# Optimization experiments

Hardware: AMD Instinct MI355X
Metric: run time of the kernel (lower is better)

The kernel has to match this reference:

```python
import jax, jax.numpy as jnp
import numpy as np

DEPTH, HEADS, DIM, MLP = 4, 8, 256, 1024
EPS = 1e-5


def setup_inputs() -> dict:
    key = jax.random.key(0)
    ks = jax.random.split(key, 12)
    s = 0.02
    return {
        "x": jax.random.normal(ks[0], (4, 2048, DIM), dtype=jnp.float32),
        "ln1_g": jnp.ones((DEPTH, DIM), jnp.float32),
        "ln1_b": jnp.zeros((DEPTH, DIM), jnp.float32),
        "w_qkv": jax.random.normal(ks[1], (DEPTH, DIM, 3 * DIM), jnp.float32) * s,
        "w_out": jax.random.normal(ks[2], (DEPTH, DIM, DIM), jnp.float32) * s,
        "b_out": jnp.zeros((DEPTH, DIM), jnp.float32),
        "ln2_g": jnp.ones((DEPTH, DIM), jnp.float32),
        "ln2_b": jnp.zeros((DEPTH, DIM), jnp.float32),
        "w1": jax.random.normal(ks[3], (DEPTH, DIM, MLP), jnp.float32) * s,
        "b1": jnp.zeros((DEPTH, MLP), jnp.float32),
        "w2": jax.random.normal(ks[4], (DEPTH, MLP, DIM), jnp.float32) * s,
        "b2": jnp.zeros((DEPTH, DIM), jnp.float32),
    }


def _layernorm(x, g, b):
    m = jnp.mean(x, axis=-1, keepdims=True)
    v = jnp.mean(jnp.square(x - m), axis=-1, keepdims=True)
    return (x - m) * jax.lax.rsqrt(v + EPS) * g + b


def _attention(x, w_qkv, w_out, b_out):
    b, n, d = x.shape
    h = HEADS
    scale = d ** (-0.5)  # NOTE: module scales by dim**-0.5, not head_dim**-0.5
    qkv = x @ w_qkv  # [b, n, 3*d]
    qkv = qkv.reshape(b, n, 3, h, d // h)
    q, k, v = jnp.moveaxis(qkv, 2, 0)  # each [b, n, h, hd]
    q = jnp.swapaxes(q, 1, 2)  # [b, h, n, hd]
    k = jnp.swapaxes(k, 1, 2)
    v = jnp.swapaxes(v, 1, 2)
    dots = jnp.einsum('bhid,bhjd->bhij', q, k) * scale
    attn = jax.nn.softmax(dots, axis=-1)
    out = jnp.einsum('bhij,bhjd->bhid', attn, v)
    out = jnp.swapaxes(out, 1, 2).reshape(b, n, d)
    return out @ w_out + b_out


def _ffn(x, w1, b1, w2, b2):
    return jax.nn.gelu(x @ w1 + b1, approximate=False) @ w2 + b2


def reference(x, ln1_g, ln1_b, w_qkv, w_out, b_out, ln2_g, ln2_b, w1, b1, w2, b2):
    for i in range(DEPTH):
        x = x + _attention(_layernorm(x, ln1_g[i], ln1_b[i]), w_qkv[i], w_out[i], b_out[i])
        x = x + _ffn(_layernorm(x, ln2_g[i], ln2_b[i]), w1[i], b1[i], w2[i], b2[i])
    return x
```

## Files before the change

### kernel.cpp

```cpp
#include <hip/hip_runtime.h>
#include <hip/hip_bf16.h>

#define DEPTH  4
#define NH     8
#define DMODEL 256
#define HD     32
#define MLPD   1024
#define SEQ    2048
#define BATCH  4
#define NTOK   (BATCH*SEQ)

typedef __attribute__((ext_vector_type(8))) short s8v;
typedef __attribute__((ext_vector_type(4))) short s4v;
typedef __attribute__((ext_vector_type(4))) float f4v;
typedef __attribute__((ext_vector_type(16))) float f16v;

#if __has_builtin(__builtin_amdgcn_exp2f)
#define EXP2(x) __builtin_amdgcn_exp2f(x)
#else
#define EXP2(x) exp2f(x)
#endif

__device__ __forceinline__ short f2bf(float f) {
    union { float f; unsigned u; } v; v.f = f;
    unsigned r = v.u + 0x7fffu + ((v.u >> 16) & 1u);
    return (short)(r >> 16);
}

__device__ __forceinline__ f4v mfma16(s8v a, s8v b, f4v c) {
    return __builtin_amdgcn_mfma_f32_16x16x32_bf16(a, b, c, 0, 0, 0);
}
__device__ __forceinline__ f16v mfma32(s8v a, s8v b, f16v c) {
    return __builtin_amdgcn_mfma_f32_32x32x16_bf16(a, b, c, 0, 0, 0);
}

__device__ __forceinline__ void glds16(const short* g, short* l) {
    __builtin_amdgcn_global_load_lds(
        (const __attribute__((address_space(1))) void*)g,
        (__attribute__((address_space(3))) void*)l, 16, 0, 0);
}

#define WAITBAR(NLIT)                                                       \
    do {                                                                    \
        __builtin_amdgcn_sched_barrier(0);                                  \
        asm volatile("s_waitcnt vmcnt(" NLIT ")" ::: "memory");             \
        __builtin_amdgcn_s_barrier();                                       \
        __builtin_amdgcn_sched_barrier(0);                                  \
    } while (0)

__global__ void transpose_cvt(const float* __restrict__ src, short* __restrict__ dst,
                              int K, int N) {
    __shared__ float tile[32][33];
    const int l = blockIdx.z;
    src += (size_t)l * K * N;
    dst += (size_t)l * N * K;
    const int n0 = blockIdx.x * 32, k0 = blockIdx.y * 32;
    const int tx = threadIdx.x, ty = threadIdx.y;
    #pragma unroll
    for (int i = 0; i < 32; i += 8)
        tile[ty + i][tx] = src[(size_t)(k0 + ty + i) * N + n0 + tx];
    __syncthreads();
    #pragma unroll
    for (int i = 0; i < 32; i += 8)
        dst[(size_t)(n0 + ty + i) * K + k0 + tx] = f2bf(tile[tx][ty + i]);
}

__global__ void ln_kernel(const float* __restrict__ x, const float* __restrict__ g,
                          const float* __restrict__ b, short* __restrict__ out) {
    const int row  = blockIdx.x * 4 + (threadIdx.x >> 6);
    const int lane = threadIdx.x & 63;
    const float4 v = *(const float4*)(x + (size_t)row * DMODEL + lane * 4);
    float s = v.x + v.y + v.z + v.w;
    #pragma unroll
    for (int m = 32; m; m >>= 1) s += __shfl_xor(s, m);
    const float mean = s * (1.0f / DMODEL);
    const float dx = v.x - mean, dy = v.y - mean, dz = v.z - mean, dw = v.w - mean;
    float q = dx*dx + dy*dy + dz*dz + dw*dw;
    #pragma unroll
    for (int m = 32; m; m >>= 1) q += __shfl_xor(q, m);
    const float rstd = rsqrtf(q * (1.0f / DMODEL) + 1e-5f);
    const float4 gg = *(const float4*)(g + lane * 4);
    const float4 bb = *(const float4*)(b + lane * 4);
    s4v o;
    o.x = f2bf(dx * rstd * gg.x + bb.x);
    o.y = f2bf(dy * rstd * gg.y + bb.y);
    o.z = f2bf(dz * rstd * gg.z + bb.z);
    o.w = f2bf(dw * rstd * gg.w + bb.w);
    *(s4v*)(out + (size_t)row * DMODEL + lane * 4) = o;
}

#define EPI_QKV  0
#define EPI_RES  1
#define EPI_GELU 2

template<int EPI>
__device__ __forceinline__ void gemm_epilogue(
        f4v acc[2][2], int trow0, int col0, int N, int g, int c,
        const float* __restrict__ bias, float* __restrict__ resio,
        short* __restrict__ outb,
        short* __restrict__ qb, short* __restrict__ kb, short* __restrict__ vtb) {
    if (EPI == EPI_QKV) {
        #pragma unroll
        for (int mf = 0; mf < 2; mf++) {
            const int tokb = trow0 + mf * 16 + g * 4;
            const int b = tokb >> 11, n = tokb & 2047;
            #pragma unroll
            for (int nf = 0; nf < 2; nf++) {
                const int colg = col0 + nf * 16 + c;
                const int part = colg >> 8, pc = colg & 255;
                const int h = pc >> 5, d = pc & 31;
                const size_t bh = (size_t)(b * NH + h);
                if (part == 2) {
                    s4v pv;
                    #pragma unroll
                    for (int r = 0; r < 4; r++) pv[r] = f2bf(acc[mf][nf][r]);
                    *(s4v*)(vtb + (bh * 32 + d) * SEQ + n) = pv;
                } else {
                    const float sc = (part == 0) ? 0.090168440f : 1.0f;
                    short* dst = (part == 0 ? qb : kb) + ((bh << 11) + n) * 32 + d;
                    #pragma unroll
                    for (int r = 0; r < 4; r++) dst[(size_t)r * 32] = f2bf(acc[mf][nf][r] * sc);
                }
            }
        }
    } else if (EPI == EPI_RES) {
        #pragma unroll
        for (int mf = 0; mf < 2; mf++)
            #pragma unroll
            for (int nf = 0; nf < 2; nf++) {
                const int colg = col0 + nf * 16 + c;
                const float bv = bias[colg];
                #pragma unroll
                for (int r = 0; r < 4; r++) {
                    const int row = trow0 + mf * 16 + g * 4 + r;
                    const size_t idx = (size_t)row * N + colg;
                    resio[idx] = resio[idx] + bv + acc[mf][nf][r];
                }
            }
    } else {
        #pragma unroll
        for (int mf = 0; mf < 2; mf++)
            #pragma unroll
            for (int nf = 0; nf < 2; nf++) {
                const int colg = col0 + nf * 16 + c;
                const float bv = bias[colg];
                #pragma unroll
                for (int r = 0; r < 4; r++) {
                    const int row = trow0 + mf * 16 + g * 4 + r;
                    const float v = acc[mf][nf][r] + bv;
                    const float ge = 0.5f * v * (1.0f + erff(v * 0.70710678118f));
                    outb[(size_t)row * N + colg] = f2bf(ge);
                }
            }
    }
}

template<int EPI>
__global__ __launch_bounds__(256) void gemm_p256(
        const short* __restrict__ A, const short* __restrict__ Bt,
        const int N, const int nbx,
        const float* __restrict__ bias,
        float* __restrict__ resio,
        short* __restrict__ outb,
        short* __restrict__ qb, short* __restrict__ kb, short* __restrict__ vtb) {
    __shared__ short ldsA[3][64 * 64];
    __shared__ short ldsB[3][64 * 64];
    const int nblk = gridDim.x;
    const int bid  = blockIdx.x;
    const int swz  = (bid & 7) * (nblk >> 3) + (bid >> 3);
    const int m0 = (swz / nbx) * 64, n0 = (swz % nbx) * 64;
    const int tid  = threadIdx.x;
    const int wave = tid >> 6, lane = tid & 63;
    const int g = lane >> 4, c = lane & 15;
    const int wm = wave >> 1, wn = wave & 1;

#define STAGEP(buf, k0)                                                     \
    do {                                                                    \
        _Pragma("unroll")                                                   \
        for (int i = 0; i < 2; i++) {                                       \
            const int idx = i * 256 + tid;                                  \
            const int row = idx >> 3, c8 = idx & 7;                         \
            const int gcol = (k0) + ((c8 ^ (row & 7)) * 8);                 \
            glds16(A  + (size_t)(m0 + row) * 256 + gcol, &ldsA[buf][idx*8]);\
            glds16(Bt + (size_t)(n0 + row) * 256 + gcol, &ldsB[buf][idx*8]);\
        }                                                                   \
    } while (0)

#define COMPUTE(buf)                                                        \
    do {                                                                    \
        _Pragma("unroll")                                                   \
        for (int kk = 0; kk < 2; kk++) {                                    \
            s8v af[2], bfr[2];                                              \
            _Pragma("unroll")                                               \
            for (int mf = 0; mf < 2; mf++)                                  \
                af[mf] = *(const s8v*)(&ldsA[buf][(wm*32+mf*16+c)*64 +      \
                                        (((kk<<2)+g) ^ (c&7)) * 8]);        \
            _Pragma("unroll")                                               \
            for (int nf = 0; nf < 2; nf++)                                  \
                bfr[nf] = *(const s8v*)(&ldsB[buf][(wn*32+nf*16+c)*64 +     \
                                        (((kk<<2)+g) ^ (c&7)) * 8]);        \
            _Pragma("unroll")                                               \
            for (int mf = 0; mf < 2; mf++)                                  \
                _Pragma("unroll")                                           \
                for (int nf = 0; nf < 2; nf++)                              \
                    acc[mf][nf] = mfma16(af[mf], bfr[nf], acc[mf][nf]);     \
        }                                                                   \
    } while (0)

    f4v acc[2][2];
    #pragma unroll
    for (int i = 0; i < 2; i++)
        #pragma unroll
        for (int j = 0; j < 2; j++) acc[i][j] = (f4v){0.f, 0.f, 0.f, 0.f};

    STAGEP(0, 0);
    STAGEP(1, 64);
    WAITBAR("4");
    STAGEP(2, 128);
    COMPUTE(0);
    WAITBAR("4");
    STAGEP(0, 192);
    COMPUTE(1);
    WAITBAR("4");
    COMPUTE(2);
    WAITBAR("0");
    COMPUTE(0);
#undef STAGEP
#undef COMPUTE

    gemm_epilogue<EPI>(acc, m0 + wm * 32, n0 + wn * 32, N, g, c,
                       bias, resio, outb, qb, kb, vtb);
}

template<int EPI>
__global__ __launch_bounds__(256) void gemm_p1024(
        const short* __restrict__ A, const short* __restrict__ Bt,
        const int N, const int nbx,
        const float* __restrict__ bias,
        float* __restrict__ resio,
        short* __restrict__ outb) {
    __shared__ short ldsA[3][64 * 64];
    __shared__ short ldsB[3][64 * 64];
    const int nblk = gridDim.x;
    const int bid  = blockIdx.x;
    const int swz  = (bid & 7) * (nblk >> 3) + (bid >> 3);
    const int m0 = (swz / nbx) * 64, n0 = (swz % nbx) * 64;
    const int tid  = threadIdx.x;
    const int wave = tid >> 6, lane = tid & 63;
    const int g = lane >> 4, c = lane & 15;
    const int wm = wave >> 1, wn = wave & 1;

#define STAGEK(buf, k0)                                                     \
    do {                                                                    \
        _Pragma("unroll")                                                   \
        for (int i = 0; i < 2; i++) {                                       \
            const int idx = i * 256 + tid;                                  \
            const int row = idx >> 3, c8 = idx & 7;                         \
            const int gcol = (k0) + ((c8 ^ (row & 7)) * 8);                 \
            glds16(A  + (size_t)(m0 + row) * 1024 + gcol, &ldsA[buf][idx*8]);\
            glds16(Bt + (size_t)(n0 + row) * 1024 + gcol, &ldsB[buf][idx*8]);\
        }                                                                   \
    } while (0)

#define COMPUTE(buf)                                                        \
    do {                                                                    \
        _Pragma("unroll")                                                   \
        for (int kk = 0; kk < 2; kk++) {                                    \
            s8v af[2], bfr[2];                                              \
            _Pragma("unroll")                                               \
            for (int mf = 0; mf < 2; mf++)                                  \
                af[mf] = *(const s8v*)(&ldsA[buf][(wm*32+mf*16+c)*64 +      \
                                        (((kk<<2)+g) ^ (c&7)) * 8]);        \
            _Pragma("unroll")                                               \
            for (int nf = 0; nf < 2; nf++)                                  \
                bfr[nf] = *(const s8v*)(&ldsB[buf][(wn*32+nf*16+c)*64 +     \
                                        (((kk<<2)+g) ^ (c&7)) * 8]);        \
            _Pragma("unroll")                                               \
            for (int mf = 0; mf < 2; mf++)                                  \
                _Pragma("unroll")                                           \
                for (int nf = 0; nf < 2; nf++)                              \
                    acc[mf][nf] = mfma16(af[mf], bfr[nf], acc[mf][nf]);     \
        }                                                                   \
    } while (0)

    f4v acc[2][2];
    #pragma unroll
    for (int i = 0; i < 2; i++)
        #pragma unroll
        for (int j = 0; j < 2; j++) acc[i][j] = (f4v){0.f, 0.f, 0.f, 0.f};

    STAGEK(0, 0);
    STAGEK(1, 64);
    WAITBAR("4");
    int b0 = 0, b1 = 1, b2 = 2;
    for (int t = 0; t < 16; ++t) {
        if (t + 2 < 16) STAGEK(b2, (t + 2) * 64);
        COMPUTE(b0);
        if (t + 2 < 16)      WAITBAR("4");
        else if (t == 14)    WAITBAR("0");
        const int tmp = b0; b0 = b1; b1 = b2; b2 = tmp;
    }
#undef STAGEK
#undef COMPUTE

    gemm_epilogue<EPI>(acc, m0 + wm * 32, n0 + wn * 32, N, g, c,
                       bias, resio, outb, nullptr, nullptr, nullptr);
}

__global__ __launch_bounds__(256) void attn_kernel(
        const short* __restrict__ qb, const short* __restrict__ kb,
        const short* __restrict__ vtb, short* __restrict__ out) {
    __shared__ short ldsK[3][4096];
    __shared__ short ldsV[3][4096];
    const int bh = blockIdx.y;
    const int tid = threadIdx.x;
    const int wave = tid >> 6, lane = tid & 63;
    const int ql = lane & 31;
    const int h2 = lane >> 5;
    const int q0 = blockIdx.x * 128 + wave * 32;
    const short* Q  = qb  + (size_t)bh * SEQ * HD;
    const short* Kp = kb  + (size_t)bh * SEQ * HD;
    const short* Vt = vtb + (size_t)bh * HD * SEQ;

    const s8v qf1 = *(const s8v*)(Q + (size_t)(q0 + ql) * HD + 8 * h2);
    const s8v qf2 = *(const s8v*)(Q + (size_t)(q0 + ql) * HD + 16 + 8 * h2);
    const s8v ones = (s8v){0x3F80,0x3F80,0x3F80,0x3F80,0x3F80,0x3F80,0x3F80,0x3F80};

    const f16v zero = {};
    f16v o   = zero;
    f16v lsv = zero;

    const short* gK = Kp + (size_t)(tid & 63) * HD + (tid >> 6) * 8;
    const short* gV = Vt + (size_t)(tid & 31) * SEQ + (tid >> 5) * 8;

#define ASTAGE(buf, kt)                                                     \
    do {                                                                    \
        glds16(gK + (size_t)(kt) * HD,        &ldsK[buf][tid * 8]);         \
        glds16(gK + (size_t)((kt) + 64) * HD, &ldsK[buf][(256 + tid) * 8]); \
        glds16(gV + (kt),                     &ldsV[buf][tid * 8]);         \
        glds16(gV + (kt) + 64,                &ldsV[buf][(256 + tid) * 8]); \
    } while (0)

#define ATILE(buf, ti)                                                      \
    do {                                                                    \
        _Pragma("unroll")                                                   \
        for (int kk = 0; kk < 2; kk++) {                                    \
            const s8v ka1 = *(const s8v*)(&ldsK[buf][((ti)*256 + kk*32 + ql + 64*h2) * 8]);        \
            const s8v ka2 = *(const s8v*)(&ldsK[buf][((ti)*256 + kk*32 + ql + 128 + 64*h2) * 8]);  \
            f16v s_ = mfma32(ka1, qf1, zero);                               \
            s_ = mfma32(ka2, qf2, s_);                                      \
            float pr_[16];                                                  \
            _Pragma("unroll")                                               \
            for (int r = 0; r < 16; r++) pr_[r] = EXP2(s_[r]);              \
            int w_[8];                                                      \
            _Pragma("unroll")                                               \
            for (int i = 0; i < 8; i++)                                     \
                asm("v_cvt_pk_bf16_f32 %0, %1, %2"                          \
                    : "=v"(w_[i]) : "v"(pr_[2*i]), "v"(pr_[2*i+1]));        \
            asm("v_permlane32_swap_b32 %0, %1" : "+v"(w_[0]), "+v"(w_[2])); \
            asm("v_permlane32_swap_b32 %0, %1" : "+v"(w_[1]), "+v"(w_[3])); \
            asm("v_permlane32_swap_b32 %0, %1" : "+v"(w_[4]), "+v"(w_[6])); \
            asm("v_permlane32_swap_b32 %0, %1" : "+v"(w_[5]), "+v"(w_[7])); \
            union { int i[4]; s8v v; } B1_, B2_;                            \
            B1_.i[0]=w_[0]; B1_.i[1]=w_[1]; B1_.i[2]=w_[2]; B1_.i[3]=w_[3]; \
            B2_.i[0]=w_[4]; B2_.i[1]=w_[5]; B2_.i[2]=w_[6]; B2_.i[3]=w_[7]; \
            lsv = mfma32(ones, B1_.v, lsv);                                 \
            lsv = mfma32(ones, B2_.v, lsv);                                 \
            const s8v va1 = *(const s8v*)(&ldsV[buf][((ti)*256 + ql + 128*kk + 32*h2) * 8]);       \
            const s8v va2 = *(const s8v*)(&ldsV[buf][((ti)*256 + ql + 128*kk + 64 + 32*h2) * 8]);  \
            o = mfma32(va1, B1_.v, o);                                      \
            o = mfma32(va2, B2_.v, o);                                      \
        }                                                                   \
    } while (0)

    ASTAGE(0, 0);
    ASTAGE(1, 128);
    WAITBAR("4");
    #pragma unroll
    for (int ph = 0; ph < 16; ++ph) {
        const int cbuf = ph % 3;
        const int nbuf = (ph + 2) % 3;
        if (ph + 2 < 16) ASTAGE(nbuf, (ph + 2) * 128);
        ATILE(cbuf, 0);
        ATILE(cbuf, 1);
        if (ph + 2 < 16)      WAITBAR("4");
        else if (ph == 14)    WAITBAR("0");
    }
#undef ASTAGE
#undef ATILE

    const int b = bh >> 3, hh = bh & 7;
    const float inv = 1.0f / lsv[0];
    const size_t rowoff = (size_t)(b * SEQ + q0 + ql) * DMODEL + hh * HD;
    #pragma unroll
    for (int rr = 0; rr < 4; rr++) {
        union { int i[2]; s4v v; } uo;
        const float e0 = o[4*rr]   * inv, e1 = o[4*rr+1] * inv;
        const float e2 = o[4*rr+2] * inv, e3 = o[4*rr+3] * inv;
        asm("v_cvt_pk_bf16_f32 %0, %1, %2" : "=v"(uo.i[0]) : "v"(e0), "v"(e1));
        asm("v_cvt_pk_bf16_f32 %0, %1, %2" : "=v"(uo.i[1]) : "v"(e2), "v"(e3));
        *(s4v*)(out + rowoff + 8 * rr + 4 * h2) = uo.v;
    }
}

extern "C" void kernel_launch(void* const* d_in, const int* in_sizes, int n_in,
                              void* d_out, int out_size, void* d_ws, size_t ws_size,
                              hipStream_t stream) {
    const float* w_qkv = (const float*)d_in[3];
    const float* w_out = (const float*)d_in[4];
    const float* b_out = (const float*)d_in[5];
    const float* w1    = (const float*)d_in[8];
    const float* b1    = (const float*)d_in[9];
    const float* w2    = (const float*)d_in[10];
    const float* b2    = (const float*)d_in[11];
    const float* ln1_g = (const float*)d_in[1];
    const float* ln1_b = (const float*)d_in[2];
    const float* ln2_g = (const float*)d_in[6];
    const float* ln2_b = (const float*)d_in[7];
    float* xout = (float*)d_out;

    short* ws    = (short*)d_ws;
    short* xn    = ws;
    short* qb    = xn    + (size_t)NTOK * DMODEL;
    short* kb    = qb    + (size_t)BATCH * NH * SEQ * HD;
    short* vtb   = kb    + (size_t)BATCH * NH * SEQ * HD;
    short* ao    = vtb   + (size_t)BATCH * NH * SEQ * HD;
    short* mid   = ao    + (size_t)NTOK * DMODEL;
    short* wqkvT = mid   + (size_t)NTOK * MLPD;
    short* woutT = wqkvT + (size_t)DEPTH * 3 * DMODEL * DMODEL;
    short* w1T   = woutT + (size_t)DEPTH * DMODEL * DMODEL;
    short* w2T   = w1T   + (size_t)DEPTH * MLPD * DMODEL;

    hipMemcpyAsync(d_out, d_in[0], (size_t)NTOK * DMODEL * sizeof(float),
                   hipMemcpyDeviceToDevice, stream);

    transpose_cvt<<<dim3(3*DMODEL/32, DMODEL/32, DEPTH), dim3(32, 8), 0, stream>>>(
        w_qkv, wqkvT, DMODEL, 3*DMODEL);
    transpose_cvt<<<dim3(DMODEL/32, DMODEL/32, DEPTH), dim3(32, 8), 0, stream>>>(
        w_out, woutT, DMODEL, DMODEL);
    transpose_cvt<<<dim3(MLPD/32, DMODEL/32, DEPTH), dim3(32, 8), 0, stream>>>(
        w1, w1T, DMODEL, MLPD);
    transpose_cvt<<<dim3(DMODEL/32, MLPD/32, DEPTH), dim3(32, 8), 0, stream>>>(
        w2, w2T, MLPD, DMODEL);

    for (int l = 0; l < DEPTH; l++) {
        ln_kernel<<<NTOK/4, 256, 0, stream>>>(xout, ln1_g + l*DMODEL, ln1_b + l*DMODEL, xn);
        gemm_p256<EPI_QKV><<<1536, 256, 0, stream>>>(
            xn, wqkvT + (size_t)l * 3 * DMODEL * DMODEL,
            3*DMODEL, 12, nullptr, nullptr, nullptr, qb, kb, vtb);
        attn_kernel<<<dim3(SEQ/128, BATCH*NH), 256, 0, stream>>>(qb, kb, vtb, ao);
        gemm_p256<EPI_RES><<<512, 256, 0, stream>>>(
            ao, woutT + (size_t)l * DMODEL * DMODEL,
            DMODEL, 4, b_out + l*DMODEL, xout, nullptr, nullptr, nullptr, nullptr);
        ln_kernel<<<NTOK/4, 256, 0, stream>>>(xout, ln2_g + l*DMODEL, ln2_b + l*DMODEL, xn);
        gemm_p256<EPI_GELU><<<2048, 256, 0, stream>>>(
            xn, w1T + (size_t)l * MLPD * DMODEL,
            MLPD, 16, b1 + l*MLPD, nullptr, mid, nullptr, nullptr, nullptr);
        gemm_p1024<EPI_RES><<<512, 256, 0, stream>>>(
            mid, w2T + (size_t)l * DMODEL * MLPD,
            DMODEL, 4, b2 + l*DMODEL, xout, nullptr);
    }
}
```

Measured before the change: 355.5 us.

## Split attention over key range into two partial passes with merge kernel

The attention kernel now splits each query block's key sequence in half along a third grid dimension. Each half writes unnormalized fp32 partial outputs and row sums to workspace, and a new merge kernel combines them and writes the bf16 attention output. This doubles the block count (512 to 1024) to fill more compute units, and shrinks LDS staging to double-buffering. The cost is an extra kernel launch, extra fp32 global traffic, and less prefetch overlap per block. The merge relies on softmax without a running max, so the partial sums share the same scale.

After: 384.8 us. 8.3% more time.

```diff
diff --git a/kernel.cpp b/kernel.cpp
--- a/kernel.cpp
+++ b/kernel.cpp
@@ -309,15 +309,18 @@
 
 __global__ __launch_bounds__(256) void attn_kernel(
         const short* __restrict__ qb, const short* __restrict__ kb,
-        const short* __restrict__ vtb, short* __restrict__ out) {
-    __shared__ short ldsK[3][4096];
-    __shared__ short ldsV[3][4096];
+        const short* __restrict__ vtb,
+        float* __restrict__ po, float* __restrict__ pl) {
+    __shared__ short ldsK[2][4096];
+    __shared__ short ldsV[2][4096];
     const int bh = blockIdx.y;
+    const int split = blockIdx.z;
     const int tid = threadIdx.x;
     const int wave = tid >> 6, lane = tid & 63;
     const int ql = lane & 31;
     const int h2 = lane >> 5;
     const int q0 = blockIdx.x * 128 + wave * 32;
+    const int klo = split * (SEQ / 2);
     const short* Q  = qb  + (size_t)bh * SEQ * HD;
     const short* Kp = kb  + (size_t)bh * SEQ * HD;
     const short* Vt = vtb + (size_t)bh * HD * SEQ;
@@ -373,34 +376,39 @@
         }                                                                   \
     } while (0)
 
-    ASTAGE(0, 0);
-    ASTAGE(1, 128);
-    WAITBAR("4");
-    #pragma unroll
-    for (int ph = 0; ph < 16; ++ph) {
-        const int cbuf = ph % 3;
-        const int nbuf = (ph + 2) % 3;
-        if (ph + 2 < 16) ASTAGE(nbuf, (ph + 2) * 128);
-        ATILE(cbuf, 0);
-        ATILE(cbuf, 1);
-        if (ph + 2 < 16)      WAITBAR("4");
-        else if (ph == 14)    WAITBAR("0");
+    ASTAGE(0, klo);
+    WAITBAR("0");
+    #pragma unroll
+    for (int ph = 0; ph < 8; ++ph) {
+        if (ph + 1 < 8) ASTAGE((ph + 1) & 1, klo + (ph + 1) * 128);
+        ATILE(ph & 1, 0);
+        ATILE(ph & 1, 1);
+        if (ph + 1 < 8) WAITBAR("0");
     }
 #undef ASTAGE
 #undef ATILE
 
-    const int b = bh >> 3, hh = bh & 7;
-    const float inv = 1.0f / lsv[0];
-    const size_t rowoff = (size_t)(b * SEQ + q0 + ql) * DMODEL + hh * HD;
+    float* pob = po + (((size_t)split * 32 + bh) * SEQ + q0 + ql) * HD;
     #pragma unroll
     for (int rr = 0; rr < 4; rr++) {
-        union { int i[2]; s4v v; } uo;
-        const float e0 = o[4*rr]   * inv, e1 = o[4*rr+1] * inv;
-        const float e2 = o[4*rr+2] * inv, e3 = o[4*rr+3] * inv;
-        asm("v_cvt_pk_bf16_f32 %0, %1, %2" : "=v"(uo.i[0]) : "v"(e0), "v"(e1));
-        asm("v_cvt_pk_bf16_f32 %0, %1, %2" : "=v"(uo.i[1]) : "v"(e2), "v"(e3));
-        *(s4v*)(out + rowoff + 8 * rr + 4 * h2) = uo.v;
+        const f4v pv = (f4v){o[4*rr], o[4*rr+1], o[4*rr+2], o[4*rr+3]};
+        *(f4v*)(pob + 8 * rr + 4 * h2) = pv;
     }
+    if (lane < 32) pl[((size_t)split * 32 + bh) * SEQ + q0 + ql] = lsv[0];
+}
+
+__global__ __launch_bounds__(256) void attn_merge(
+        const float* __restrict__ po, const float* __restrict__ pl,
+        short* __restrict__ ao) {
+    const int t = threadIdx.x;
+    const int q = blockIdx.x * 8 + (t >> 5);
+    const int d = t & 31;
+    const int bh = blockIdx.y, b = bh >> 3, h = bh & 7;
+    const size_t i0 = ((size_t)bh * SEQ + q) * HD + d;
+    const size_t i1 = ((size_t)(32 + bh) * SEQ + q) * HD + d;
+    const float ov = po[i0] + po[i1];
+    const float l  = pl[(size_t)bh * SEQ + q] + pl[(size_t)(32 + bh) * SEQ + q];
+    ao[((size_t)(b * SEQ + q)) * DMODEL + h * HD + d] = f2bf(ov / l);
 }
 
 extern "C" void kernel_launch(void* const* d_in, const int* in_sizes, int n_in,
@@ -430,6 +438,8 @@
     short* woutT = wqkvT + (size_t)DEPTH * 3 * DMODEL * DMODEL;
     short* w1T   = woutT + (size_t)DEPTH * DMODEL * DMODEL;
     short* w2T   = w1T   + (size_t)DEPTH * MLPD * DMODEL;
+    float* po    = (float*)(w2T + (size_t)DEPTH * DMODEL * MLPD);
+    float* pl    = po + (size_t)2 * 32 * SEQ * HD;
 
     hipMemcpyAsync(d_out, d_in[0], (size_t)NTOK * DMODEL * sizeof(float),
                    hipMemcpyDeviceToDevice, stream);
@@ -448,7 +458,8 @@
         gemm_p256<EPI_QKV><<<1536, 256, 0, stream>>>(
             xn, wqkvT + (size_t)l * 3 * DMODEL * DMODEL,
             3*DMODEL, 12, nullptr, nullptr, nullptr, qb, kb, vtb);
-        attn_kernel<<<dim3(SEQ/128, BATCH*NH), 256, 0, stream>>>(qb, kb, vtb, ao);
+        attn_kernel<<<dim3(SEQ/128, BATCH*NH, 2), 256, 0, stream>>>(qb, kb, vtb, po, pl);
+        attn_merge<<<dim3(SEQ/8, BATCH*NH), 256, 0, stream>>>(po, pl, ao);
         gemm_p256<EPI_RES><<<512, 256, 0, stream>>>(
             ao, woutT + (size_t)l * DMODEL * DMODEL,
             DMODEL, 4, b_out + l*DMODEL, xout, nullptr, nullptr, nullptr, nullptr);
```
